# Kernel tuning notes

Hardware: AMD Instinct MI355X
Metric: run time of the kernel (lower is better)

The kernel has to match this reference:

```python
import jax, jax.numpy as jnp
import numpy as np

VOCAB, EMB, UNITS, B, S = 32000, 256, 512, 32, 512


def _lstm_scan(x_bse, h0, c0, W, U, b):
    """Keras-order LSTM (gates i,f,g,o). x_bse: [B,S,E]. Returns (out [B,S,U], hT, cT)."""
    # Precompute input projections for all timesteps: [B,S,4U] -> [S,B,4U]
    zx = jnp.einsum('bse,eu->bsu', x_bse, W) + b
    zx = jnp.swapaxes(zx, 0, 1)

    def step(carry, zt):
        h, c = carry
        z = zt + h @ U  # [B,4U]
        i, f, g, o = jnp.split(z, 4, axis=-1)
        i = jax.nn.sigmoid(i)
        f = jax.nn.sigmoid(f)
        g = jnp.tanh(g)
        o = jax.nn.sigmoid(o)
        c = f * c + i * g
        h = o * jnp.tanh(c)
        return (h, c), h

    (hT, cT), hs = jax.lax.scan(step, (h0, c0), zx)
    return jnp.swapaxes(hs, 0, 1), hT, cT


def setup_inputs() -> dict:
    key = jax.random.key(0)
    ks = jax.random.split(key, 8)
    g = 0.05
    inp = {
        'x': jax.random.randint(ks[0], (B, S), 0, VOCAB),
        'fh': jnp.zeros((B, UNITS), jnp.float32),
        'fc': jnp.zeros((B, UNITS), jnp.float32),
        'bh': jnp.zeros((B, UNITS), jnp.float32),
        'bc': jnp.zeros((B, UNITS), jnp.float32),
        'emb': jax.random.normal(ks[1], (VOCAB, EMB), jnp.float32) * g,
        'Wf': jax.random.normal(ks[2], (EMB, 4 * UNITS), jnp.float32) * g,
        'Uf': jax.random.normal(ks[3], (UNITS, 4 * UNITS), jnp.float32) * g,
        'bf': jnp.zeros((4 * UNITS,), jnp.float32),
        'Wb': jax.random.normal(ks[4], (EMB, 4 * UNITS), jnp.float32) * g,
        'Ub': jax.random.normal(ks[5], (UNITS, 4 * UNITS), jnp.float32) * g,
        'bb': jnp.zeros((4 * UNITS,), jnp.float32),
    }
    return inp


def reference(x, fh, fc, bh, bc, emb, Wf, Uf, bf, Wb, Ub, bb):
    xe = emb[x]  # [B,S,E] embedding lookup
    # Forward direction
    out_f, fhT, fcT = _lstm_scan(xe, fh, fc, Wf, Uf, bf)
    # Backward direction: process reversed sequence, then re-reverse outputs
    out_b_rev, bhT, bcT = _lstm_scan(xe[:, ::-1, :], bh, bc, Wb, Ub, bb)
    out_b = out_b_rev[:, ::-1, :]
    output = jnp.concatenate([out_f, out_b], axis=-1)  # [B,S,2U]
    return output, fhT, fcT, bhT, bcT
```

## Files before the change

kernel.cpp:

```cpp
#include <hip/hip_runtime.h>

#define SEQ   512
#define BATCH 32
#define EMBD  256
#define UNITS 512
#define G4    2048
#define NW1   128
#define NW2   32
#define UPW   16
#define HSTR  520
#define NTHR  512

typedef short  short8 __attribute__((ext_vector_type(8)));
typedef float  f32x4  __attribute__((ext_vector_type(4)));
typedef unsigned int u32x4 __attribute__((ext_vector_type(4)));
typedef unsigned int u32x2 __attribute__((ext_vector_type(2)));

static constexpr unsigned long long ZX2_OFF   = 0ull;
static constexpr unsigned long long ZX2_BYTES = 2ull * SEQ * NW1 * BATCH * 16 * 2;
static constexpr unsigned long long HB_OFF    = ZX2_OFF + ZX2_BYTES;
static constexpr unsigned long long HB_BYTES  = 2ull * SEQ * BATCH * UNITS * 2;
static constexpr unsigned long long FLG_OFF   = HB_OFF + HB_BYTES;
static constexpr unsigned long long FLG_BYTES = 2ull * NW2 * 4;

__device__ __forceinline__ unsigned short f2bf(float f) {
  unsigned int u = __float_as_uint(f);
  u = (u + 0x7FFFu + ((u >> 16) & 1u)) >> 16;
  return (unsigned short)u;
}
__device__ __forceinline__ float bf2f(unsigned short s) {
  return __uint_as_float(((unsigned int)s) << 16);
}
__device__ __forceinline__ unsigned sent2(unsigned w) {
  return (unsigned)(((w & 0xFFFFu) == 0xFFFFu) | ((w >> 16) == 0xFFFFu));
}
__device__ __forceinline__ unsigned chk4(u32x4 g) {
  return sent2(g[0]) | sent2(g[1]) | sent2(g[2]) | sent2(g[3]);
}

__global__ __launch_bounds__(256)
void k_zx(const int* __restrict__ x, const float* __restrict__ emb,
          const float* __restrict__ Wf, const float* __restrict__ bf,
          const float* __restrict__ Wb, const float* __restrict__ bb,
          unsigned short* __restrict__ zx2)
{
  const int nb  = blockIdx.x;
  const int mb  = blockIdx.y;
  const int dir = blockIdx.z;
  const float* __restrict__ W    = dir ? Wb : Wf;
  const float* __restrict__ bias = dir ? bb : bf;
  const int tid = threadIdx.x;
  const int M0 = mb * 64, N0 = nb * 64;

  __shared__ __align__(16) float Ast[32][68];
  __shared__ __align__(16) float Bs [32][68];
  __shared__ int tok[64];

  if (tid < 64) {
    int m = M0 + tid;
    int t = m >> 5, b = m & 31;
    int s = dir ? (SEQ - 1 - t) : t;
    tok[tid] = x[b * SEQ + s];
  }

  float acc[4][4];
  #pragma unroll
  for (int r = 0; r < 4; ++r)
    #pragma unroll
    for (int c = 0; c < 4; ++c) acc[r][c] = 0.f;

  const int mq = tid >> 4, nq = tid & 15;

  for (int kb = 0; kb < 8; ++kb) {
    __syncthreads();
    {
      int m = tid >> 2, q = tid & 3;
      const float* src = emb + (size_t)tok[m] * EMBD + kb * 32 + q * 8;
      float4 v0 = *(const float4*)src;
      float4 v1 = *(const float4*)(src + 4);
      int k0 = q * 8;
      Ast[k0+0][m] = v0.x; Ast[k0+1][m] = v0.y; Ast[k0+2][m] = v0.z; Ast[k0+3][m] = v0.w;
      Ast[k0+4][m] = v1.x; Ast[k0+5][m] = v1.y; Ast[k0+6][m] = v1.z; Ast[k0+7][m] = v1.w;
    }
    {
      int k = tid >> 3, q = tid & 7;
      const float* src = W + (size_t)(kb*32 + k) * G4 + N0 + q * 8;
      float4 w0 = *(const float4*)src;
      float4 w1 = *(const float4*)(src + 4);
      *(float4*)&Bs[k][q*8]     = w0;
      *(float4*)&Bs[k][q*8 + 4] = w1;
    }
    __syncthreads();
    #pragma unroll 8
    for (int k = 0; k < 32; ++k) {
      float4 a  = *(const float4*)&Ast[k][mq*4];
      float4 bv = *(const float4*)&Bs[k][nq*4];
      acc[0][0] += a.x*bv.x; acc[0][1] += a.x*bv.y; acc[0][2] += a.x*bv.z; acc[0][3] += a.x*bv.w;
      acc[1][0] += a.y*bv.x; acc[1][1] += a.y*bv.y; acc[1][2] += a.y*bv.z; acc[1][3] += a.y*bv.w;
      acc[2][0] += a.z*bv.x; acc[2][1] += a.z*bv.y; acc[2][2] += a.z*bv.z; acc[2][3] += a.z*bv.w;
      acc[3][0] += a.w*bv.x; acc[3][1] += a.w*bv.y; acc[3][2] += a.w*bv.z; acc[3][3] += a.w*bv.w;
    }
  }

  float4 bs4 = *(const float4*)(bias + N0 + nq*4);
  const int g = N0 >> 9;
  const int u = (N0 & 511) + nq * 4;
  const int w = u >> 2;
  #pragma unroll
  for (int r = 0; r < 4; ++r) {
    int m = M0 + mq*4 + r;
    int t = m >> 5, b = m & 31;
    unsigned short p0 = f2bf(acc[r][0] + bs4.x);
    unsigned short p1 = f2bf(acc[r][1] + bs4.y);
    unsigned short p2 = f2bf(acc[r][2] + bs4.z);
    unsigned short p3 = f2bf(acc[r][3] + bs4.w);
    uint2 pk;
    pk.x = (unsigned)p0 | ((unsigned)p1 << 16);
    pk.y = (unsigned)p2 | ((unsigned)p3 << 16);
    size_t off = ((((size_t)dir*SEQ + t)*NW1 + w)*BATCH + b)*16 + g*4;
    *(uint2*)(zx2 + off) = pk;
  }
}

__global__ __launch_bounds__(NTHR, 2)
void k_rec2(const float* __restrict__ fh, const float* __restrict__ fc,
            const float* __restrict__ bh, const float* __restrict__ bc,
            const float* __restrict__ Uf, const float* __restrict__ Ub,
            const unsigned short* __restrict__ zx2,
            unsigned short* __restrict__ hring_all,
            int* __restrict__ claim,
            float* __restrict__ out)
{
  const int tid = threadIdx.x;
  __shared__ int s_slot, s_loc;

  if (tid == 0) {
    unsigned xcc;
    asm volatile("s_getreg_b32 %0, hwreg(HW_REG_XCC_ID)" : "=s"(xcc));
    int slot = -1;
    if (xcc < 2) {
      int base = (int)xcc * NW2;
      for (int i = 0; i < NW2 && slot < 0; ++i)
        if (atomicCAS(&claim[base + i], 0, 1) == 0) slot = base + i;
    }
    if (slot < 0) {
      for (int sp = 0; sp < 96; ++sp) __builtin_amdgcn_s_sleep(8);
      for (int i = 0; i < 2 * NW2 && slot < 0; ++i)
        if (atomicCAS(&claim[i], 0, 1) == 0) slot = i;
    }
    s_slot = slot;
    s_loc  = (slot >= 0 && (unsigned)(slot >> 5) == xcc) ? 1 : 0;
  }
  __syncthreads();
  const int slot = s_slot;
  if (slot < 0) return;
  const int loc = s_loc;
  const int dir = slot >> 5;
  const int w   = slot & (NW2 - 1);
  const int u0  = w * UPW;
  const int l   = tid & 63;
  const int wid = tid >> 6;
  const int mt  = wid & 1;
  const int ct  = wid >> 1;

  const float* __restrict__ U  = dir ? Ub : Uf;
  const float* __restrict__ h0 = dir ? bh : fh;
  const float* __restrict__ c0 = dir ? bc : fc;

  __shared__ __align__(16) unsigned short hs[BATCH * HSTR];

  unsigned short* __restrict__ hring = hring_all + (size_t)dir * SEQ * BATCH * UNITS;
  const unsigned short* __restrict__ zxd =
      zx2 + ((size_t)dir * SEQ) * (NW1 * BATCH * 16);

  const int krow = (l >> 4) * 8;
  const size_t gcol = (size_t)((l & 15) >> 2) * 512 + u0 + ct * 4 + (l & 3);
  short8 uhi[16], ulo[16];
  #pragma unroll
  for (int s = 0; s < 16; ++s) {
    const float* up = U + (size_t)(s * 32 + krow) * G4 + gcol;
    short8 hi8, lo8;
    #pragma unroll
    for (int j = 0; j < 8; ++j) {
      float uv = up[(size_t)j * G4];
      unsigned short h16 = f2bf(uv);
      float rem = uv - bf2f(h16);
      hi8[j] = (short)h16;
      lo8[j] = (short)f2bf(rem);
    }
    uhi[s] = hi8; ulo[s] = lo8;
  }

  float c_old[4];
  #pragma unroll
  for (int r = 0; r < 4; ++r) {
    int b_r = 16 * mt + (l >> 4) * 4 + r;
    c_old[r] = c0[(size_t)b_r * UNITS + u0 + ct * 4 + (l & 3)];
  }

  {
    int r = tid >> 4, cq = tid & 15;
    const float* src = h0 + (size_t)r * UNITS;
    #pragma unroll
    for (int i = 0; i < 4; ++i) {
      int c = i * 16 + cq;
      float4 v0 = *(const float4*)(src + c * 8);
      float4 v1 = *(const float4*)(src + c * 8 + 4);
      short8 pk;
      pk[0]=(short)f2bf(v0.x); pk[1]=(short)f2bf(v0.y);
      pk[2]=(short)f2bf(v0.z); pk[3]=(short)f2bf(v0.w);
      pk[4]=(short)f2bf(v1.x); pk[5]=(short)f2bf(v1.y);
      pk[6]=(short)f2bf(v1.z); pk[7]=(short)f2bf(v1.w);
      *(short8*)(&hs[r * HSTR + c * 8]) = pk;
    }
  }
  __syncthreads();

  const int arow  = 16 * mt + (l & 15);
  const unsigned short* hsrow = hs + arow * HSTR;
  const int agrp0 = l >> 4;
  const int sr = tid >> 4, scq = tid & 15;
  unsigned short* const hs_dst = hs + sr * HSTR + scq * 8;
  const bool isg = ((l & 15) >> 2) == 2;
  const float An = isg ? 2.f : 1.f;
  const float Cn = isg ? -1.f : 0.f;
  const float Bn = isg ? -2.f : -1.f;
  const size_t ZXT = (size_t)NW1 * BATCH * 16;
  const size_t zbase = ((size_t)(4 * w + ct) * BATCH + 16 * mt + (l >> 4) * 4) * 16
                       + ((l & 15) >> 2) * 4 + (l & 3);

  for (int t = 0; t < SEQ; ++t) {
    unsigned short zxr[4];
    #pragma unroll
    for (int r = 0; r < 4; ++r) zxr[r] = zxd[(size_t)t * ZXT + zbase + r * 16];

    if (t > 0) {
      const unsigned short* src =
          hring + ((size_t)(t - 1) * BATCH + sr) * UNITS + scq * 8;
      u32x4 g0, g1, g2, g3;
      asm volatile("global_load_dwordx4 %0, %1, off sc0"            : "=&v"(g0) : "v"(src) : "memory");
      asm volatile("global_load_dwordx4 %0, %1, off offset:256 sc0" : "=&v"(g1) : "v"(src) : "memory");
      asm volatile("global_load_dwordx4 %0, %1, off offset:512 sc0" : "=&v"(g2) : "v"(src) : "memory");
      asm volatile("global_load_dwordx4 %0, %1, off offset:768 sc0" : "=&v"(g3) : "v"(src) : "memory");
      asm volatile("s_waitcnt vmcnt(0)" : "+v"(g0), "+v"(g1), "+v"(g2), "+v"(g3));
      __builtin_amdgcn_sched_barrier(0);
      unsigned b0 = chk4(g0), b1 = chk4(g1), b2 = chk4(g2), b3 = chk4(g3);
      int guard = 0;
      while ((b0 | b1 | b2 | b3) && ++guard < (1 << 20)) {
        __builtin_amdgcn_s_sleep(1);
        if (guard & 1) {
          if (b0) asm volatile("global_load_dwordx4 %0, %1, off sc0 sc1"            : "=&v"(g0) : "v"(src) : "memory");
          if (b1) asm volatile("global_load_dwordx4 %0, %1, off offset:256 sc0 sc1" : "=&v"(g1) : "v"(src) : "memory");
          if (b2) asm volatile("global_load_dwordx4 %0, %1, off offset:512 sc0 sc1" : "=&v"(g2) : "v"(src) : "memory");
          if (b3) asm volatile("global_load_dwordx4 %0, %1, off offset:768 sc0 sc1" : "=&v"(g3) : "v"(src) : "memory");
        } else {
          if (b0) asm volatile("global_load_dwordx4 %0, %1, off sc0"            : "=&v"(g0) : "v"(src) : "memory");
          if (b1) asm volatile("global_load_dwordx4 %0, %1, off offset:256 sc0" : "=&v"(g1) : "v"(src) : "memory");
          if (b2) asm volatile("global_load_dwordx4 %0, %1, off offset:512 sc0" : "=&v"(g2) : "v"(src) : "memory");
          if (b3) asm volatile("global_load_dwordx4 %0, %1, off offset:768 sc0" : "=&v"(g3) : "v"(src) : "memory");
        }
        asm volatile("s_waitcnt vmcnt(0)" : "+v"(g0), "+v"(g1), "+v"(g2), "+v"(g3));
        __builtin_amdgcn_sched_barrier(0);
        b0 = chk4(g0); b1 = chk4(g1); b2 = chk4(g2); b3 = chk4(g3);
      }
      *(u32x4*)(hs_dst      ) = g0;
      *(u32x4*)(hs_dst + 128) = g1;
      *(u32x4*)(hs_dst + 256) = g2;
      *(u32x4*)(hs_dst + 384) = g3;
      __syncthreads();
    }

    f32x4 accA = {0.f, 0.f, 0.f, 0.f};
    f32x4 accB = {0.f, 0.f, 0.f, 0.f};
    #pragma unroll
    for (int s = 0; s < 16; ++s) {
      short8 a = *(const short8*)(hsrow + (4 * s + agrp0) * 8);
      accA = __builtin_amdgcn_mfma_f32_16x16x32_bf16(a, uhi[s], accA, 0, 0, 0);
      accB = __builtin_amdgcn_mfma_f32_16x16x32_bf16(a, ulo[s], accB, 0, 0, 0);
    }

    float vv[4];
    #pragma unroll
    for (int r = 0; r < 4; ++r) {
      float z = accA[r] + accB[r] + bf2f(zxr[r]);
      float e = __expf(Bn * z);
      vv[r] = An * __builtin_amdgcn_rcpf(1.f + e) + Cn;
    }
    float hn[4], cn[4];
    unsigned pk0[4], pk1[4];
    #pragma unroll
    for (int r = 0; r < 4; ++r) {
      float wv = __shfl_xor(vv[r], 8);
      float x1 = __shfl_xor(vv[r], 4);
      float x2 = __shfl_xor(wv,    4);
      cn[r] = x1 * c_old[r] + vv[r] * wv;
      c_old[r] = cn[r];
      float e2 = __expf(-2.f * cn[r]);
      float th = 2.f * __builtin_amdgcn_rcpf(1.f + e2) - 1.f;
      hn[r] = x2 * th;
      unsigned hb = (unsigned)f2bf(hn[r]);
      unsigned d  = (hb & 0xFFFFu) | (__shfl_xor((int)hb, 1) << 16);
      unsigned d2 = (unsigned)__shfl_xor((int)d, 2);
      pk0[r] = d; pk1[r] = d2;
    }

    if ((l & 15) == 0) {
      #pragma unroll
      for (int r = 0; r < 4; ++r) {
        int b_r = 16 * mt + (l >> 4) * 4 + r;
        unsigned short* dst = hring + ((size_t)t * BATCH + b_r) * UNITS + u0 + ct * 4;
        u32x2 pk; pk[0] = pk0[r]; pk[1] = pk1[r];
        if (loc)
          asm volatile("global_store_dwordx2 %0, %1, off sc0"
                       :: "v"(dst), "v"(pk) : "memory");
        else
          asm volatile("global_store_dwordx2 %0, %1, off sc0 sc1"
                       :: "v"(dst), "v"(pk) : "memory");
      }
    }

    if ((l & 15) < 4) {
      int sidx = dir ? (SEQ - 1 - t) : t;
      #pragma unroll
      for (int r = 0; r < 4; ++r) {
        int b_r = 16 * mt + (l >> 4) * 4 + r;
        size_t oi = ((size_t)b_r * SEQ + sidx) * 1024 + dir * 512 + u0 + ct * 4 + (l & 3);
        __builtin_nontemporal_store(hn[r], &out[oi]);
      }
      if (t == SEQ - 1) {
        size_t base = (size_t)BATCH * SEQ * 1024;
        #pragma unroll
        for (int r = 0; r < 4; ++r) {
          int b_r = 16 * mt + (l >> 4) * 4 + r;
          size_t o1 = base + (size_t)(2*dir  ) * BATCH * UNITS + (size_t)b_r * UNITS + u0 + ct * 4 + (l & 3);
          size_t o2 = base + (size_t)(2*dir+1) * BATCH * UNITS + (size_t)b_r * UNITS + u0 + ct * 4 + (l & 3);
          __builtin_nontemporal_store(hn[r], &out[o1]);
          __builtin_nontemporal_store(cn[r], &out[o2]);
        }
      }
    }
  }
}

extern "C" void kernel_launch(void* const* d_in, const int* in_sizes, int n_in,
                              void* d_out, int out_size, void* d_ws, size_t ws_size,
                              hipStream_t stream)
{
  const int*   x   = (const int*)  d_in[0];
  const float* fh  = (const float*)d_in[1];
  const float* fc  = (const float*)d_in[2];
  const float* bh  = (const float*)d_in[3];
  const float* bc  = (const float*)d_in[4];
  const float* emb = (const float*)d_in[5];
  const float* Wf  = (const float*)d_in[6];
  const float* Uf  = (const float*)d_in[7];
  const float* bf  = (const float*)d_in[8];
  const float* Wb  = (const float*)d_in[9];
  const float* Ub  = (const float*)d_in[10];
  const float* bb  = (const float*)d_in[11];
  float* out = (float*)d_out;

  if (ws_size < FLG_OFF + FLG_BYTES) return;

  unsigned short* zx2   = (unsigned short*)((char*)d_ws + ZX2_OFF);
  unsigned short* hring = (unsigned short*)((char*)d_ws + HB_OFF);
  int*            claim = (int*)((char*)d_ws + FLG_OFF);

  hipMemsetAsync(hring, 0xFF, HB_BYTES, stream);
  hipMemsetAsync(claim, 0, FLG_BYTES, stream);
  k_zx  <<<dim3(32, 256, 2), 256, 0, stream>>>(x, emb, Wf, bf, Wb, bb, zx2);
  k_rec2<<<dim3(256), NTHR, 0, stream>>>(fh, fc, bh, bc, Uf, Ub, zx2, hring, claim, out);
}
```

Baseline: 2.061 ms.

## Add per-step producer flags for recurrent h exchange and prefetch next zx

Each workgroup now publishes a per-timestep ready flag after its h stores. Consumers poll the 32 flags of the previous step with one load per lane, then read the h ring, instead of spinning on sentinel values in the h data itself. The zx input for the next step is also loaded one iteration ahead, so its latency overlaps the current step. This adds an extra global round trip and a vmcnt wait per step. It also relies on store ordering between the h writes and the flag write, which a wrong vmcnt count could break.

```diff
diff --git a/kernel.cpp b/kernel.cpp
--- a/kernel.cpp
+++ b/kernel.cpp
@@ -21,7 +21,9 @@
 static constexpr unsigned long long HB_OFF    = ZX2_OFF + ZX2_BYTES;
 static constexpr unsigned long long HB_BYTES  = 2ull * SEQ * BATCH * UNITS * 2;
 static constexpr unsigned long long FLG_OFF   = HB_OFF + HB_BYTES;
-static constexpr unsigned long long FLG_BYTES = 2ull * NW2 * 4;
+static constexpr unsigned long long FLG_BYTES = 4096;
+static constexpr unsigned long long SF_OFF    = FLG_OFF + FLG_BYTES;
+static constexpr unsigned long long SF_BYTES  = 2ull * SEQ * NW2 * 4;
 
 __device__ __forceinline__ unsigned short f2bf(float f) {
   unsigned int u = __float_as_uint(f);
@@ -128,7 +130,7 @@
             const float* __restrict__ Uf, const float* __restrict__ Ub,
             const unsigned short* __restrict__ zx2,
             unsigned short* __restrict__ hring_all,
-            int* __restrict__ claim,
+            int* __restrict__ claim, int* __restrict__ sflag,
             float* __restrict__ out)
 {
   const int tid = threadIdx.x;
@@ -170,6 +172,7 @@
   __shared__ __align__(16) unsigned short hs[BATCH * HSTR];
 
   unsigned short* __restrict__ hring = hring_all + (size_t)dir * SEQ * BATCH * UNITS;
+  int* __restrict__ flg = sflag + (size_t)dir * SEQ * NW2;
   const unsigned short* __restrict__ zxd =
       zx2 + ((size_t)dir * SEQ) * (NW1 * BATCH * 16);
 
@@ -229,12 +232,28 @@
   const size_t zbase = ((size_t)(4 * w + ct) * BATCH + 16 * mt + (l >> 4) * 4) * 16
                        + ((l & 15) >> 2) * 4 + (l & 3);
 
+  unsigned short zx_cur[4];
+  #pragma unroll
+  for (int r = 0; r < 4; ++r) zx_cur[r] = zxd[zbase + r * 16];
+
   for (int t = 0; t < SEQ; ++t) {
-    unsigned short zxr[4];
-    #pragma unroll
-    for (int r = 0; r < 4; ++r) zxr[r] = zxd[(size_t)t * ZXT + zbase + r * 16];
-
     if (t > 0) {
+      asm volatile("s_waitcnt vmcnt(0)" ::: "memory");
+      {
+        const int* fpl = flg + (size_t)(t - 1) * NW2 + (l & 31);
+        unsigned v; int guard = 0;
+        for (;;) {
+          if ((guard & 3) == 3)
+            asm volatile("global_load_dword %0, %1, off sc0 sc1\n\ts_waitcnt vmcnt(0)"
+                         : "=v"(v) : "v"(fpl) : "memory");
+          else
+            asm volatile("global_load_dword %0, %1, off sc0\n\ts_waitcnt vmcnt(0)"
+                         : "=v"(v) : "v"(fpl) : "memory");
+          __builtin_amdgcn_sched_barrier(0);
+          if (__ballot(v != 0) == ~0ull || ++guard >= (1 << 20)) break;
+          __builtin_amdgcn_s_sleep(1);
+        }
+      }
       const unsigned short* src =
           hring + ((size_t)(t - 1) * BATCH + sr) * UNITS + scq * 8;
       u32x4 g0, g1, g2, g3;
@@ -282,7 +301,7 @@
     float vv[4];
     #pragma unroll
     for (int r = 0; r < 4; ++r) {
-      float z = accA[r] + accB[r] + bf2f(zxr[r]);
+      float z = accA[r] + accB[r] + bf2f(zx_cur[r]);
       float e = __expf(Bn * z);
       vv[r] = An * __builtin_amdgcn_rcpf(1.f + e) + Cn;
     }
@@ -304,20 +323,31 @@
       pk0[r] = d; pk1[r] = d2;
     }
 
-    if ((l & 15) == 0) {
+    if (t < SEQ - 1) {
+      if ((l & 15) == 0) {
+        #pragma unroll
+        for (int r = 0; r < 4; ++r) {
+          int b_r = 16 * mt + (l >> 4) * 4 + r;
+          unsigned short* dst = hring + ((size_t)t * BATCH + b_r) * UNITS + u0 + ct * 4;
+          u32x2 pk; pk[0] = pk0[r]; pk[1] = pk1[r];
+          if (loc)
+            asm volatile("global_store_dwordx2 %0, %1, off sc0"
+                         :: "v"(dst), "v"(pk) : "memory");
+          else
+            asm volatile("global_store_dwordx2 %0, %1, off sc0 sc1"
+                         :: "v"(dst), "v"(pk) : "memory");
+        }
+      }
+    }
+    __builtin_amdgcn_sched_barrier(0);
+
+    unsigned short zx_nxt[4] = {0, 0, 0, 0};
+    if (t + 1 < SEQ) {
       #pragma unroll
-      for (int r = 0; r < 4; ++r) {
-        int b_r = 16 * mt + (l >> 4) * 4 + r;
-        unsigned short* dst = hring + ((size_t)t * BATCH + b_r) * UNITS + u0 + ct * 4;
-        u32x2 pk; pk[0] = pk0[r]; pk[1] = pk1[r];
-        if (loc)
-          asm volatile("global_store_dwordx2 %0, %1, off sc0"
-                       :: "v"(dst), "v"(pk) : "memory");
-        else
-          asm volatile("global_store_dwordx2 %0, %1, off sc0 sc1"
-                       :: "v"(dst), "v"(pk) : "memory");
-      }
-    }
+      for (int r = 0; r < 4; ++r)
+        zx_nxt[r] = zxd[(size_t)(t + 1) * ZXT + zbase + r * 16];
+    }
+    __builtin_amdgcn_sched_barrier(0);
 
     if ((l & 15) < 4) {
       int sidx = dir ? (SEQ - 1 - t) : t;
@@ -339,6 +369,24 @@
         }
       }
     }
+    __builtin_amdgcn_sched_barrier(0);
+
+    if (t < SEQ - 1) {
+      asm volatile("s_waitcnt vmcnt(8)" ::: "memory");
+      if (tid == 0) {
+        int* fdst = flg + (size_t)t * NW2 + w;
+        unsigned one = 1u;
+        if (loc)
+          asm volatile("global_store_dword %0, %1, off sc0"
+                       :: "v"(fdst), "v"(one) : "memory");
+        else
+          asm volatile("global_store_dword %0, %1, off sc0 sc1"
+                       :: "v"(fdst), "v"(one) : "memory");
+      }
+    }
+
+    #pragma unroll
+    for (int r = 0; r < 4; ++r) zx_cur[r] = zx_nxt[r];
   }
 }
 
@@ -360,14 +408,15 @@
   const float* bb  = (const float*)d_in[11];
   float* out = (float*)d_out;
 
-  if (ws_size < FLG_OFF + FLG_BYTES) return;
+  if (ws_size < SF_OFF + SF_BYTES) return;
 
   unsigned short* zx2   = (unsigned short*)((char*)d_ws + ZX2_OFF);
   unsigned short* hring = (unsigned short*)((char*)d_ws + HB_OFF);
   int*            claim = (int*)((char*)d_ws + FLG_OFF);
+  int*            sflag = (int*)((char*)d_ws + SF_OFF);
 
   hipMemsetAsync(hring, 0xFF, HB_BYTES, stream);
-  hipMemsetAsync(claim, 0, FLG_BYTES, stream);
+  hipMemsetAsync(claim, 0, FLG_BYTES + SF_BYTES, stream);
   k_zx  <<<dim3(32, 256, 2), 256, 0, stream>>>(x, emb, Wf, bf, Wb, bb, zx2);
-  k_rec2<<<dim3(256), NTHR, 0, stream>>>(fh, fc, bh, bc, Uf, Ub, zx2, hring, claim, out);
-}
+  k_rec2<<<dim3(256), NTHR, 0, stream>>>(fh, fc, bh, bc, Uf, Ub, zx2, hring, claim, sflag, out);
+}
```

Result: faster. 1.918 ms (-6.9%).
